# Kernel tuning notes

Measured on AMD Instinct MI355X. Metric: run time of the kernel, lower is better.

Reference implementation:

```python
import jax, jax.numpy as jnp
import numpy as np

IS_CAUSAL = True
NEG_INF = float('-inf')


def setup_inputs() -> dict:
    key = jax.random.key(0)
    kq, kk, kv = jax.random.split(key, 3)
    B, H, S, D = 4, 16, 2048, 64
    return {
        'query': jax.random.normal(kq, (B, H, S, D), dtype=jnp.float32),
        'key': jax.random.normal(kk, (B, H, S, D), dtype=jnp.float32),
        'value': jax.random.normal(kv, (B, H, S, D), dtype=jnp.float32),
    }


def reference(query, key, value):
    # Attention(Q,K,V) = softmax(QK^T / sqrt(d_k) + causal_mask) V
    d_k = query.shape[-1]
    scale = 1.0 / np.sqrt(d_k).astype(np.float32)
    # [B,H,Sq,Sk]
    scores = jnp.einsum('bhqd,bhkd->bhqk', query, key) * scale
    if IS_CAUSAL:
        sq, sk = query.shape[-2], key.shape[-2]
        causal = jnp.triu(jnp.ones((sq, sk), dtype=bool), k=1)
        scores = jnp.where(causal[None, None, :, :], NEG_INF, scores)
    weights = jax.nn.softmax(scores, axis=-1)
    # dropout p=0.0 (eval): identity
    out = jnp.einsum('bhqk,bhkd->bhqd', weights, value)
    return out
```

## Files before the change

kernel.cpp:

```cpp
#include <hip/hip_runtime.h>
#include <stdint.h>


#define SLEN 2048
#define DHEAD 64
#define NHEADS 64
#define NELEM (SLEN * DHEAD * NHEADS)
#define PADP 72

typedef short bf16x8 __attribute__((ext_vector_type(8)));
typedef float f32x4 __attribute__((ext_vector_type(4)));

__device__ __forceinline__ uint32_t pkbf(float hi, float lo) {
    uint32_t a = __builtin_bit_cast(uint32_t, lo) + 0x8000u;
    uint32_t b = __builtin_bit_cast(uint32_t, hi) + 0x8000u;
    return __builtin_amdgcn_perm(b, a, 0x07060302u);
}
__device__ __forceinline__ unsigned short f2bf(float f) {
    return (unsigned short)((__builtin_bit_cast(uint32_t, f) + 0x8000u) >> 16);
}
__device__ __forceinline__ int swz(int row, int g) {
    return row * 64 + ((g ^ (row & 7)) << 3);
}

__global__ __launch_bounds__(256)
void convert_prep(const float* __restrict__ K, const float* __restrict__ V,
                  unsigned short* __restrict__ Kb, unsigned short* __restrict__ Vtb) {
    __shared__ unsigned short Lt[64 * 264];
    const int b = blockIdx.x, t = threadIdx.x;
    if (b < 4096) {
        const int off = (b * 256 + t) * 8;
        float4 a = *(const float4*)(K + off);
        float4 c = *(const float4*)(K + off + 4);
        uint4 o;
        o.x = pkbf(a.y, a.x); o.y = pkbf(a.w, a.z);
        o.z = pkbf(c.y, c.x); o.w = pkbf(c.w, c.z);
        *(uint4*)(Kb + off) = o;
    } else {
        const int vb2 = b - 4096;
        const int head = vb2 >> 3, kblk = vb2 & 7;
        const float* Vh = V + (size_t)head * (SLEN * DHEAD) + kblk * 256 * DHEAD;
        unsigned short* Vo = Vtb + (size_t)head * (SLEN * DHEAD) + kblk * 256;
#pragma unroll
        for (int i = 0; i < 16; ++i) {
            int idx = t + 256 * i;
            int key = idx >> 4, d4 = idx & 15;
            float4 v = *(const float4*)(Vh + key * DHEAD + d4 * 4);
            Lt[(d4 * 4 + 0) * 264 + key] = f2bf(v.x);
            Lt[(d4 * 4 + 1) * 264 + key] = f2bf(v.y);
            Lt[(d4 * 4 + 2) * 264 + key] = f2bf(v.z);
            Lt[(d4 * 4 + 3) * 264 + key] = f2bf(v.w);
        }
        __syncthreads();
#pragma unroll
        for (int jj = 0; jj < 8; ++jj) {
            int idx = t + 256 * jj;
            int d = idx >> 5, k8 = idx & 31;
            *(uint4*)(Vo + (size_t)d * SLEN + k8 * 8) = *(const uint4*)(Lt + d * 264 + k8 * 8);
        }
    }
}

__global__ __launch_bounds__(256, 4)
void sdpa_mfma(const float* __restrict__ Qf, const unsigned short* __restrict__ Kb,
               const unsigned short* __restrict__ Vtb, float* __restrict__ Og) {
    const int n = blockIdx.x;
    const int j = n >> 8, c = n & 255;
    const int head = c & 63;
    const int A  = (c >> 6) + 4 * j;
    const int Bq = 31 - A;

    const size_t hb = (size_t)head * SLEN * DHEAD;
    const float* Qh = Qf + hb;
    const unsigned short* Kh  = Kb + hb;
    const unsigned short* Vth = Vtb + hb;
    float* Oh = Og + hb;

    const int tid  = threadIdx.x;
    const int w    = tid >> 6, lane = tid & 63;
    const int cl   = lane & 15, quad = lane >> 4;

    __shared__ unsigned short Kl[64 * 64];
    __shared__ unsigned short Vt[64 * 64];
    __shared__ unsigned short Pl[4 * 32 * PADP];

    const int qw = ((w < 2) ? A * 64 : Bq * 64) + (w & 1) * 32;
    unsigned short* Plw = Pl + w * 32 * PADP;

    bf16x8 qf[2][2];
#pragma unroll
    for (int m = 0; m < 2; ++m)
#pragma unroll
        for (int h = 0; h < 2; ++h) {
            const float* src = Qh + (size_t)(qw + m * 16 + cl) * DHEAD + h * 32 + quad * 8;
            float4 a = *(const float4*)src;
            float4 b = *(const float4*)(src + 4);
            uint4 u;
            u.x = pkbf(a.y, a.x); u.y = pkbf(a.w, a.z);
            u.z = pkbf(b.y, b.x); u.w = pkbf(b.w, b.z);
            qf[m][h] = __builtin_bit_cast(bf16x8, u);
        }

    f32x4 o[2][4];
#pragma unroll
    for (int m = 0; m < 2; ++m)
#pragma unroll
        for (int d = 0; d < 4; ++d) o[m][d] = (f32x4){0.f, 0.f, 0.f, 0.f};
    float ls[2] = {0.f, 0.f};
    const float SCL = 0.18033688f;

    const int p1 = tid + 256;
    const int srow0 = tid >> 3, sg0 = tid & 7;
    const int srow1 = p1 >> 3,  sg1 = p1 & 7;
    const int lo0 = swz(srow0, sg0), lo1 = swz(srow1, sg1);
    const size_t kS0 = (size_t)srow0 * DHEAD + sg0 * 8, kS1 = (size_t)srow1 * DHEAD + sg1 * 8;
    const size_t vS0 = (size_t)srow0 * SLEN + sg0 * 8,  vS1 = (size_t)srow1 * SLEN + sg1 * 8;

    const int ntiles = Bq + 1;
    uint4 kr0 = *(const uint4*)(Kh + kS0), kr1 = *(const uint4*)(Kh + kS1);
    uint4 vr0 = *(const uint4*)(Vth + vS0), vr1 = *(const uint4*)(Vth + vS1);

    for (int t = 0; t < ntiles; ++t) {
        const int k0 = t * 64;
        __syncthreads();
        *(uint4*)(Kl + lo0) = kr0; *(uint4*)(Kl + lo1) = kr1;
        *(uint4*)(Vt + lo0) = vr0; *(uint4*)(Vt + lo1) = vr1;
        __syncthreads();
        if (t + 1 < ntiles) {
            const size_t ko = (size_t)(k0 + 64) * DHEAD;
            kr0 = *(const uint4*)(Kh + kS0 + ko);
            kr1 = *(const uint4*)(Kh + kS1 + ko);
            vr0 = *(const uint4*)(Vth + vS0 + (k0 + 64));
            vr1 = *(const uint4*)(Vth + vS1 + (k0 + 64));
        }
        if (k0 > qw + 31) continue;
        const bool partial = (k0 + 63 > qw);

#pragma unroll
        for (int kk = 0; kk < 4; ++kk) {
            bf16x8 kb0 = __builtin_bit_cast(bf16x8, *(const uint4*)(Kl + swz(kk * 16 + cl, quad)));
            bf16x8 kb1 = __builtin_bit_cast(bf16x8, *(const uint4*)(Kl + swz(kk * 16 + cl, 4 + quad)));
            const int krel = kk * 16 + quad * 4;
#pragma unroll
            for (int qq = 0; qq < 2; ++qq) {
                f32x4 s = (f32x4){0.f, 0.f, 0.f, 0.f};
                s = __builtin_amdgcn_mfma_f32_16x16x32_bf16(kb0, qf[qq][0], s, 0, 0, 0);
                s = __builtin_amdgcn_mfma_f32_16x16x32_bf16(kb1, qf[qq][1], s, 0, 0, 0);
                float p0, p1v, p2, p3;
                if (partial) {
                    const int qrel = qw - k0 + qq * 16 + cl;
                    p0 = (krel + 0 <= qrel) ? __builtin_amdgcn_exp2f(s[0] * SCL) : 0.f;
                    p1v = (krel + 1 <= qrel) ? __builtin_amdgcn_exp2f(s[1] * SCL) : 0.f;
                    p2 = (krel + 2 <= qrel) ? __builtin_amdgcn_exp2f(s[2] * SCL) : 0.f;
                    p3 = (krel + 3 <= qrel) ? __builtin_amdgcn_exp2f(s[3] * SCL) : 0.f;
                } else {
                    p0 = __builtin_amdgcn_exp2f(s[0] * SCL);
                    p1v = __builtin_amdgcn_exp2f(s[1] * SCL);
                    p2 = __builtin_amdgcn_exp2f(s[2] * SCL);
                    p3 = __builtin_amdgcn_exp2f(s[3] * SCL);
                }
                ls[qq] += (p0 + p1v) + (p2 + p3);
                uint2 pw;
                pw.x = pkbf(p1v, p0);
                pw.y = pkbf(p3, p2);
                *(uint2*)(Plw + (qq * 16 + cl) * PADP + kk * 16 + quad * 4) = pw;
            }
        }

        bf16x8 pa[2][2];
#pragma unroll
        for (int m = 0; m < 2; ++m)
#pragma unroll
            for (int h = 0; h < 2; ++h)
                pa[m][h] = __builtin_bit_cast(bf16x8,
                    *(const uint4*)(Plw + (m * 16 + cl) * PADP + h * 32 + quad * 8));
#pragma unroll
        for (int dd = 0; dd < 4; ++dd) {
            bf16x8 vb0 = __builtin_bit_cast(bf16x8, *(const uint4*)(Vt + swz(dd * 16 + cl, quad)));
            bf16x8 vb1 = __builtin_bit_cast(bf16x8, *(const uint4*)(Vt + swz(dd * 16 + cl, 4 + quad)));
#pragma unroll
            for (int m = 0; m < 2; ++m) {
                o[m][dd] = __builtin_amdgcn_mfma_f32_16x16x32_bf16(pa[m][0], vb0, o[m][dd], 0, 0, 0);
                o[m][dd] = __builtin_amdgcn_mfma_f32_16x16x32_bf16(pa[m][1], vb1, o[m][dd], 0, 0, 0);
            }
        }
    }

#pragma unroll
    for (int qq = 0; qq < 2; ++qq) {
        float v = ls[qq];
        v += __shfl_xor(v, 16);
        v += __shfl_xor(v, 32);
        ls[qq] = v;
    }

#pragma unroll
    for (int m = 0; m < 2; ++m)
#pragma unroll
        for (int r = 0; r < 4; ++r) {
            const float inv = 1.0f / __shfl(ls[m], quad * 4 + r);
#pragma unroll
            for (int dd = 0; dd < 4; ++dd)
                Oh[(size_t)(qw + m * 16 + quad * 4 + r) * DHEAD + dd * 16 + cl] = o[m][dd][r] * inv;
        }
}

extern "C" void kernel_launch(void* const* d_in, const int* in_sizes, int n_in,
                              void* d_out, int out_size, void* d_ws, size_t ws_size,
                              hipStream_t stream) {
    const float* Q = (const float*)d_in[0];
    const float* K = (const float*)d_in[1];
    const float* V = (const float*)d_in[2];
    float*       O = (float*)d_out;

    unsigned short* Kbf  = (unsigned short*)d_ws;
    unsigned short* Vtbf = Kbf + NELEM;

    convert_prep<<<dim3(4096 + 512), dim3(256), 0, stream>>>(K, V, Kbf, Vtbf);
    sdpa_mfma<<<dim3(1024), dim3(256), 0, stream>>>(Q, Kbf, Vtbf, O);
}
```

Before: 196.5 us.

## Keep P in registers via 16x16x16 MFMA, double-buffer K/V LDS, prescale Q

The P tile now feeds the PV product straight from the QK accumulator registers through 16x16x16 bf16 MFMAs, which removes the per-warp LDS round-trip for P. K and V tiles are double-buffered in LDS, so each iteration needs one barrier instead of two, and global loads are issued two tiles ahead. The softmax scale is folded into Q when it is converted to bf16, which drops a multiply per score. Block-to-head mapping also changes so consecutive blocks share a head. The costs are twice as many PV MFMA instructions at half the K depth, more LDS use for the double buffers, and extra V fragment loads.

```diff
diff --git a/kernel.cpp b/kernel.cpp
--- a/kernel.cpp
+++ b/kernel.cpp
@@ -6,9 +6,9 @@
 #define DHEAD 64
 #define NHEADS 64
 #define NELEM (SLEN * DHEAD * NHEADS)
-#define PADP 72
 
 typedef short bf16x8 __attribute__((ext_vector_type(8)));
+typedef short bf16x4 __attribute__((ext_vector_type(4)));
 typedef float f32x4 __attribute__((ext_vector_type(4)));
 
 __device__ __forceinline__ uint32_t pkbf(float hi, float lo) {
@@ -21,6 +21,14 @@
 }
 __device__ __forceinline__ int swz(int row, int g) {
     return row * 64 + ((g ^ (row & 7)) << 3);
+}
+__device__ __forceinline__ f32x4 mfma16(bf16x4 a, bf16x4 b, f32x4 c) {
+#if __has_builtin(__builtin_amdgcn_mfma_f32_16x16x16bf16_1k)
+    return __builtin_amdgcn_mfma_f32_16x16x16bf16_1k(a, b, c, 0, 0, 0);
+#else
+    asm volatile("v_mfma_f32_16x16x16_bf16 %0, %1, %2, %0" : "+v"(c) : "v"(a), "v"(b));
+    return c;
+#endif
 }
 
 __global__ __launch_bounds__(256)
@@ -65,28 +73,28 @@
 void sdpa_mfma(const float* __restrict__ Qf, const unsigned short* __restrict__ Kb,
                const unsigned short* __restrict__ Vtb, float* __restrict__ Og) {
     const int n = blockIdx.x;
-    const int j = n >> 8, c = n & 255;
-    const int head = c & 63;
-    const int A  = (c >> 6) + 4 * j;
-    const int Bq = 31 - A;
+    const int head = n >> 4;
+    const int A = n & 15;
+    const int Bt = 31 - A;
 
     const size_t hb = (size_t)head * SLEN * DHEAD;
     const float* Qh = Qf + hb;
-    const unsigned short* Kh  = Kb + hb;
+    const unsigned short* Kh = Kb + hb;
     const unsigned short* Vth = Vtb + hb;
     float* Oh = Og + hb;
 
-    const int tid  = threadIdx.x;
-    const int w    = tid >> 6, lane = tid & 63;
-    const int cl   = lane & 15, quad = lane >> 4;
-
-    __shared__ unsigned short Kl[64 * 64];
-    __shared__ unsigned short Vt[64 * 64];
-    __shared__ unsigned short Pl[4 * 32 * PADP];
-
-    const int qw = ((w < 2) ? A * 64 : Bq * 64) + (w & 1) * 32;
-    unsigned short* Plw = Pl + w * 32 * PADP;
-
+    const int tid = threadIdx.x;
+    const int w = tid >> 6, lane = tid & 63;
+    const int cl = lane & 15, quad = lane >> 4;
+
+    __shared__ unsigned short Kl[2][64 * 64];
+    __shared__ unsigned short Vl[2][64 * 64];
+
+    const int mytile = (w < 2) ? A : Bt;
+    const int qw = mytile * 64 + (w & 1) * 32;
+    const int qrb = (w & 1) * 32;
+
+    const float SCL = 0.18033688f;
     bf16x8 qf[2][2];
 #pragma unroll
     for (int m = 0; m < 2; ++m)
@@ -96,8 +104,8 @@
             float4 a = *(const float4*)src;
             float4 b = *(const float4*)(src + 4);
             uint4 u;
-            u.x = pkbf(a.y, a.x); u.y = pkbf(a.w, a.z);
-            u.z = pkbf(b.y, b.x); u.w = pkbf(b.w, b.z);
+            u.x = pkbf(a.y * SCL, a.x * SCL); u.y = pkbf(a.w * SCL, a.z * SCL);
+            u.z = pkbf(b.y * SCL, b.x * SCL); u.w = pkbf(b.w * SCL, b.z * SCL);
             qf[m][h] = __builtin_bit_cast(bf16x8, u);
         }
 
@@ -107,81 +115,87 @@
 #pragma unroll
         for (int d = 0; d < 4; ++d) o[m][d] = (f32x4){0.f, 0.f, 0.f, 0.f};
     float ls[2] = {0.f, 0.f};
-    const float SCL = 0.18033688f;
-
-    const int p1 = tid + 256;
+
+    const int s1 = tid + 256;
     const int srow0 = tid >> 3, sg0 = tid & 7;
-    const int srow1 = p1 >> 3,  sg1 = p1 & 7;
+    const int srow1 = s1 >> 3,  sg1 = s1 & 7;
     const int lo0 = swz(srow0, sg0), lo1 = swz(srow1, sg1);
     const size_t kS0 = (size_t)srow0 * DHEAD + sg0 * 8, kS1 = (size_t)srow1 * DHEAD + sg1 * 8;
     const size_t vS0 = (size_t)srow0 * SLEN + sg0 * 8,  vS1 = (size_t)srow1 * SLEN + sg1 * 8;
 
-    const int ntiles = Bq + 1;
-    uint4 kr0 = *(const uint4*)(Kh + kS0), kr1 = *(const uint4*)(Kh + kS1);
-    uint4 vr0 = *(const uint4*)(Vth + vS0), vr1 = *(const uint4*)(Vth + vS1);
+    const int ntiles = Bt + 1;
+
+    auto load_regs = [&](int t, uint4& k0r, uint4& k1r, uint4& v0r, uint4& v1r) {
+        const int j = (t < ntiles) ? t : ntiles - 1;
+        const size_t ko = (size_t)j * 64 * DHEAD;
+        k0r = *(const uint4*)(Kh + kS0 + ko);
+        k1r = *(const uint4*)(Kh + kS1 + ko);
+        v0r = *(const uint4*)(Vth + vS0 + j * 64);
+        v1r = *(const uint4*)(Vth + vS1 + j * 64);
+    };
+
+    uint4 kr0, kr1, vr0, vr1;
+    load_regs(0, kr0, kr1, vr0, vr1);
+    *(uint4*)(Kl[0] + lo0) = kr0; *(uint4*)(Kl[0] + lo1) = kr1;
+    *(uint4*)(Vl[0] + lo0) = vr0; *(uint4*)(Vl[0] + lo1) = vr1;
+    load_regs(1, kr0, kr1, vr0, vr1);
 
     for (int t = 0; t < ntiles; ++t) {
-        const int k0 = t * 64;
         __syncthreads();
-        *(uint4*)(Kl + lo0) = kr0; *(uint4*)(Kl + lo1) = kr1;
-        *(uint4*)(Vt + lo0) = vr0; *(uint4*)(Vt + lo1) = vr1;
-        __syncthreads();
+        const int bw = (t + 1) & 1;
         if (t + 1 < ntiles) {
-            const size_t ko = (size_t)(k0 + 64) * DHEAD;
-            kr0 = *(const uint4*)(Kh + kS0 + ko);
-            kr1 = *(const uint4*)(Kh + kS1 + ko);
-            vr0 = *(const uint4*)(Vth + vS0 + (k0 + 64));
-            vr1 = *(const uint4*)(Vth + vS1 + (k0 + 64));
-        }
-        if (k0 > qw + 31) continue;
-        const bool partial = (k0 + 63 > qw);
+            *(uint4*)(Kl[bw] + lo0) = kr0; *(uint4*)(Kl[bw] + lo1) = kr1;
+            *(uint4*)(Vl[bw] + lo0) = vr0; *(uint4*)(Vl[bw] + lo1) = vr1;
+        }
+        if (t + 2 < ntiles) load_regs(t + 2, kr0, kr1, vr0, vr1);
+
+        if (t * 64 > qw + 31) continue;
+        const bool partial = (t == mytile);
+        const unsigned short* Kt = Kl[t & 1];
+        const unsigned short* Vt = Vl[t & 1];
 
 #pragma unroll
         for (int kk = 0; kk < 4; ++kk) {
-            bf16x8 kb0 = __builtin_bit_cast(bf16x8, *(const uint4*)(Kl + swz(kk * 16 + cl, quad)));
-            bf16x8 kb1 = __builtin_bit_cast(bf16x8, *(const uint4*)(Kl + swz(kk * 16 + cl, 4 + quad)));
+            bf16x8 kb0 = __builtin_bit_cast(bf16x8, *(const uint4*)(Kt + swz(kk * 16 + cl, quad)));
+            bf16x8 kb1 = __builtin_bit_cast(bf16x8, *(const uint4*)(Kt + swz(kk * 16 + cl, 4 + quad)));
+            uint2 vbr[4];
+#pragma unroll
+            for (int dd = 0; dd < 4; ++dd) {
+                const int row = dd * 16 + cl;
+                const int g = kk * 2 + (quad >> 1);
+                vbr[dd] = *(const uint2*)(Vt + row * 64 + ((g ^ (row & 7)) << 3) + (quad & 1) * 4);
+            }
             const int krel = kk * 16 + quad * 4;
+            bf16x4 pa[2];
 #pragma unroll
             for (int qq = 0; qq < 2; ++qq) {
                 f32x4 s = (f32x4){0.f, 0.f, 0.f, 0.f};
                 s = __builtin_amdgcn_mfma_f32_16x16x32_bf16(kb0, qf[qq][0], s, 0, 0, 0);
                 s = __builtin_amdgcn_mfma_f32_16x16x32_bf16(kb1, qf[qq][1], s, 0, 0, 0);
-                float p0, p1v, p2, p3;
+                float p0, p1, p2, p3;
                 if (partial) {
-                    const int qrel = qw - k0 + qq * 16 + cl;
-                    p0 = (krel + 0 <= qrel) ? __builtin_amdgcn_exp2f(s[0] * SCL) : 0.f;
-                    p1v = (krel + 1 <= qrel) ? __builtin_amdgcn_exp2f(s[1] * SCL) : 0.f;
-                    p2 = (krel + 2 <= qrel) ? __builtin_amdgcn_exp2f(s[2] * SCL) : 0.f;
-                    p3 = (krel + 3 <= qrel) ? __builtin_amdgcn_exp2f(s[3] * SCL) : 0.f;
+                    const int qrel = qrb + qq * 16 + cl;
+                    p0 = (krel + 0 <= qrel) ? __builtin_amdgcn_exp2f(s[0]) : 0.f;
+                    p1 = (krel + 1 <= qrel) ? __builtin_amdgcn_exp2f(s[1]) : 0.f;
+                    p2 = (krel + 2 <= qrel) ? __builtin_amdgcn_exp2f(s[2]) : 0.f;
+                    p3 = (krel + 3 <= qrel) ? __builtin_amdgcn_exp2f(s[3]) : 0.f;
                 } else {
-                    p0 = __builtin_amdgcn_exp2f(s[0] * SCL);
-                    p1v = __builtin_amdgcn_exp2f(s[1] * SCL);
-                    p2 = __builtin_amdgcn_exp2f(s[2] * SCL);
-                    p3 = __builtin_amdgcn_exp2f(s[3] * SCL);
+                    p0 = __builtin_amdgcn_exp2f(s[0]);
+                    p1 = __builtin_amdgcn_exp2f(s[1]);
+                    p2 = __builtin_amdgcn_exp2f(s[2]);
+                    p3 = __builtin_amdgcn_exp2f(s[3]);
                 }
-                ls[qq] += (p0 + p1v) + (p2 + p3);
+                ls[qq] += (p0 + p1) + (p2 + p3);
                 uint2 pw;
-                pw.x = pkbf(p1v, p0);
+                pw.x = pkbf(p1, p0);
                 pw.y = pkbf(p3, p2);
-                *(uint2*)(Plw + (qq * 16 + cl) * PADP + kk * 16 + quad * 4) = pw;
+                pa[qq] = __builtin_bit_cast(bf16x4, pw);
             }
-        }
-
-        bf16x8 pa[2][2];
-#pragma unroll
-        for (int m = 0; m < 2; ++m)
-#pragma unroll
-            for (int h = 0; h < 2; ++h)
-                pa[m][h] = __builtin_bit_cast(bf16x8,
-                    *(const uint4*)(Plw + (m * 16 + cl) * PADP + h * 32 + quad * 8));
-#pragma unroll
-        for (int dd = 0; dd < 4; ++dd) {
-            bf16x8 vb0 = __builtin_bit_cast(bf16x8, *(const uint4*)(Vt + swz(dd * 16 + cl, quad)));
-            bf16x8 vb1 = __builtin_bit_cast(bf16x8, *(const uint4*)(Vt + swz(dd * 16 + cl, 4 + quad)));
-#pragma unroll
-            for (int m = 0; m < 2; ++m) {
-                o[m][dd] = __builtin_amdgcn_mfma_f32_16x16x32_bf16(pa[m][0], vb0, o[m][dd], 0, 0, 0);
-                o[m][dd] = __builtin_amdgcn_mfma_f32_16x16x32_bf16(pa[m][1], vb1, o[m][dd], 0, 0, 0);
+#pragma unroll
+            for (int dd = 0; dd < 4; ++dd) {
+                const bf16x4 vbf = __builtin_bit_cast(bf16x4, vbr[dd]);
+                o[0][dd] = mfma16(pa[0], vbf, o[0][dd]);
+                o[1][dd] = mfma16(pa[1], vbf, o[1][dd]);
             }
         }
     }
@@ -193,7 +207,6 @@
         v += __shfl_xor(v, 32);
         ls[qq] = v;
     }
-
 #pragma unroll
     for (int m = 0; m < 2; ++m)
 #pragma unroll
```

After: 220.7 us. +12.3%, slower.
